# Optimization experiments

Hardware: AMD Instinct MI355X
Metric: run time of the kernel (lower is better)

Reference implementation:

```python
import jax, jax.numpy as jnp
import numpy as np

H, C = 4, 128            # heads, per-head channels (GATConv(in, 128, heads=4))
HC = H * C               # 512
NEG_SLOPE = 0.2          # PyG GATConv default LeakyReLU slope
EPS_BN = 1e-5


def gat_conv(x, src, dst, W, a_src, a_dst, b, n_nodes):
    # x: [N, F_in], W: [F_in, H*C], a_src/a_dst: [H, C], b: [H*C]
    h = (x @ W).reshape(n_nodes, H, C)                       # [N,H,C]
    al_s = jnp.einsum('nhc,hc->nh', h, a_src)                # [N,H]
    al_d = jnp.einsum('nhc,hc->nh', h, a_dst)                # [N,H]
    e = jax.nn.leaky_relu(al_s[src] + al_d[dst], NEG_SLOPE)  # [E,H] per-edge logits
    m = jax.ops.segment_max(e, dst, num_segments=n_nodes)    # stable segment softmax
    p = jnp.exp(e - m[dst])
    s = jax.ops.segment_sum(p, dst, num_segments=n_nodes)
    alpha = p / (s[dst] + 1e-16)                             # [E,H]
    out = jax.ops.segment_sum(h[src] * alpha[:, :, None], dst, num_segments=n_nodes)
    return out.reshape(n_nodes, HC) + b                      # concat heads + bias


def batch_norm(x, g, b):
    mu = x.mean(0)
    var = x.var(0)  # biased, as torch BatchNorm1d uses for normalization
    return (x - mu) * jax.lax.rsqrt(var + EPS_BN) * g + b


def setup_inputs() -> dict:
    N, E, F_IN, OUT = 20000, 256000, 128, 10
    key = jax.random.key(0)
    ks = jax.random.split(key, 40)
    sc = 0.05
    inp = {
        'x': jax.random.normal(ks[0], (N, F_IN), dtype=jnp.float32),
        'edge_index': jax.random.randint(ks[1], (2, E), 0, N, dtype=jnp.int64) if jax.config.jax_enable_x64 else jax.random.randint(ks[1], (2, E), 0, N).astype(jnp.int32),
        'batch': jnp.zeros((N,), dtype=jnp.int32),
    }
    k = 2
    fin = F_IN
    for i in range(1, 5):
        inp[f'W{i}'] = jax.random.normal(ks[k], (fin, HC), dtype=jnp.float32) * sc; k += 1
        inp[f'as{i}'] = jax.random.normal(ks[k], (H, C), dtype=jnp.float32) * sc; k += 1
        inp[f'ad{i}'] = jax.random.normal(ks[k], (H, C), dtype=jnp.float32) * sc; k += 1
        inp[f'b{i}'] = jnp.zeros((HC,), dtype=jnp.float32)
        inp[f'g{i}'] = jnp.ones((HC,), dtype=jnp.float32)
        inp[f'bt{i}'] = jnp.zeros((HC,), dtype=jnp.float32)
        fin = HC
    inp['lw1'] = jax.random.normal(ks[k], (HC, 128), dtype=jnp.float32) * sc; k += 1
    inp['lb1'] = jnp.zeros((128,), dtype=jnp.float32)
    inp['lw2'] = jax.random.normal(ks[k], (128, 64), dtype=jnp.float32) * sc; k += 1
    inp['lb2'] = jnp.zeros((64,), dtype=jnp.float32)
    inp['lw3'] = jax.random.normal(ks[k], (64, OUT), dtype=jnp.float32) * sc; k += 1
    inp['lb3'] = jnp.zeros((OUT,), dtype=jnp.float32)
    return inp


def reference(x, edge_index, batch,
              W1, as1, ad1, b1, g1, bt1,
              W2, as2, ad2, b2, g2, bt2,
              W3, as3, ad3, b3, g3, bt3,
              W4, as4, ad4, b4, g4, bt4,
              lw1, lb1, lw2, lb2, lw3, lb3):
    n = x.shape[0]
    # add self-loops (PyG GATConv default add_self_loops=True)
    loops = jnp.arange(n, dtype=edge_index.dtype)
    src = jnp.concatenate([edge_index[0], loops])
    dst = jnp.concatenate([edge_index[1], loops])

    h = jax.nn.elu(gat_conv(x, src, dst, W1, as1, ad1, b1, n))
    h = batch_norm(h, g1, bt1)
    h = jax.nn.elu(gat_conv(h, src, dst, W2, as2, ad2, b2, n))
    h = batch_norm(h, g2, bt2)
    h = jax.nn.elu(gat_conv(h, src, dst, W3, as3, ad3, b3, n))
    h = batch_norm(h, g3, bt3)
    h = jax.nn.elu(gat_conv(h, src, dst, W4, as4, ad4, b4, n))
    h = batch_norm(h, g4, bt4)

    h = jax.nn.relu(h @ lw1 + lb1)   # dropout is identity in eval
    h = jax.nn.relu(h @ lw2 + lb2)
    return jax.nn.log_softmax(h @ lw3 + lb3, axis=-1)
```

## Files before the change

### kernel.cpp

```cpp
#include <hip/hip_runtime.h>
#include <hip/hip_bf16.h>
#include <math.h>

#define HC 512
#define NHEAD 4
#define NEG_SLOPE 0.2f
#define EPS_BN 1e-5f

typedef __attribute__((ext_vector_type(8))) _Float16 half8;
typedef __attribute__((ext_vector_type(4))) _Float16 half4v;
typedef __attribute__((ext_vector_type(4))) float f32x4;

#define GLOAD16(gptr, lptr)                                                      \
    __builtin_amdgcn_global_load_lds(                                            \
        (const __attribute__((address_space(1))) unsigned int*)(gptr),           \
        (__attribute__((address_space(3))) unsigned int*)(lptr), 16, 0, 0)

__global__ void hist_kernel(const int* __restrict__ dstE, int* __restrict__ cnt,
                            int E, int N) {
    int i = blockIdx.x * 256 + threadIdx.x;
    if (i < E + N) {
        int d = (i < E) ? dstE[i] : (i - E);
        atomicAdd(&cnt[d], 1);
    }
}

__global__ __launch_bounds__(1024) void scan_kernel(int* __restrict__ rowptr,
                                                    int* __restrict__ wr, int n) {
    __shared__ int wsum[16];
    __shared__ int carry_s;
    int t = threadIdx.x, lane = t & 63, wv = t >> 6;
    if (t == 0) carry_s = 0;
    __syncthreads();
    for (int base = 0; base < n; base += 1024) {
        int v = (base + t < n) ? rowptr[base + t] : 0;
        int x = v;
#pragma unroll
        for (int off = 1; off < 64; off <<= 1) {
            int y = __shfl_up(x, off);
            if (lane >= off) x += y;
        }
        if (lane == 63) wsum[wv] = x;
        __syncthreads();
        if (wv == 0) {
            int s = (lane < 16) ? wsum[lane] : 0;
#pragma unroll
            for (int off = 1; off < 16; off <<= 1) {
                int y = __shfl_up(s, off);
                if (lane >= off) s += y;
            }
            if (lane < 16) wsum[lane] = s;
        }
        __syncthreads();
        int woff = (wv == 0) ? 0 : wsum[wv - 1];
        int tot = wsum[15];
        int carry = carry_s;
        if (base + t < n) {
            int excl = carry + woff + x - v;
            rowptr[base + t] = excl;
            wr[base + t] = excl;
        }
        __syncthreads();
        if (t == 1023) carry_s = carry + tot;
        __syncthreads();
    }
    if (threadIdx.x == 0) rowptr[n] = carry_s;
}

__global__ void scatter_kernel(const int* __restrict__ srcE,
                               const int* __restrict__ dstE,
                               int* __restrict__ wr, int* __restrict__ csrc,
                               int E, int N) {
    int i = blockIdx.x * 256 + threadIdx.x;
    if (i < E + N) {
        int d = (i < E) ? dstE[i] : (i - E);
        int s = (i < E) ? srcE[i] : (i - E);
        int p = atomicAdd(&wr[d], 1);
        csrc[p] = s;
    }
}

__global__ __launch_bounds__(256) void advec_kernel(const double* __restrict__ stats,
                                                    const float* __restrict__ g,
                                                    const float* __restrict__ bt,
                                                    float* __restrict__ avec,
                                                    float* __restrict__ dvec,
                                                    double invN) {
    int k = blockIdx.x * 256 + threadIdx.x;
    if (k >= HC) return;
    double mu = stats[k] * invN;
    double var = stats[HC + k] * invN - mu * mu;
    float a = g[k] * (float)rsqrt(var + (double)EPS_BN);
    avec[k] = a;
    dvec[k] = bt[k] - (float)mu * a;
}

__global__ __launch_bounds__(256) void wsplit_kernel(const float* __restrict__ W,
                                                     const float* __restrict__ avec,
                                                     _Float16* __restrict__ hiT,
                                                     int K, int Nc) {
    __shared__ float tile[32][33];
    int bx = blockIdx.x * 32;
    int by = blockIdx.y * 32;
    int tx = threadIdx.x & 31, ty = threadIdx.x >> 5;
#pragma unroll
    for (int r = 0; r < 32; r += 8)
        tile[ty + r][tx] = W[(size_t)(by + ty + r) * Nc + bx + tx];
    __syncthreads();
    int k = by + tx;
    float a = avec ? avec[k] : 1.f;
#pragma unroll
    for (int r = 0; r < 32; r += 8) {
        int n = bx + ty + r;
        hiT[(size_t)n * K + k] = (_Float16)(tile[tx][ty + r] * a);
    }
}

__global__ __launch_bounds__(256) void bvec_kernel(const float* __restrict__ W,
                                                   const float* __restrict__ dvec,
                                                   const float* __restrict__ extra,
                                                   float* __restrict__ bvec,
                                                   int K, int Nc) {
    int wv = (blockIdx.x * 256 + threadIdx.x) >> 6;
    int lane = threadIdx.x & 63;
    if (wv >= Nc) return;
    float s = 0.f;
    for (int k = lane; k < K; k += 64)
        s = fmaf(dvec[k], W[(size_t)k * Nc + wv], s);
#pragma unroll
    for (int off = 32; off; off >>= 1) s += __shfl_xor(s, off);
    if (lane == 0) bvec[wv] = s + (extra ? extra[wv] : 0.f);
}

__global__ __launch_bounds__(256) void xcvt_kernel(const float* __restrict__ x,
                                                   _Float16* __restrict__ xh, int total) {
    for (int i = blockIdx.x * 256 + threadIdx.x; i < total; i += gridDim.x * 256)
        xh[i] = (_Float16)x[i];
}

template <int EPI>
__global__ __launch_bounds__(256) void mfma_gemm(const _Float16* __restrict__ A,
                                                 const _Float16* __restrict__ BT,
                                                 const float* __restrict__ bvec,
                                                 _Float16* __restrict__ H16,
                                                 float* __restrict__ C,
                                                 int M, int K, int Nc) {
    __shared__ _Float16 sm[2 * 4096];
    _Float16* sA = sm;
    _Float16* sB = sm + 4096;

    const int nwg = gridDim.x * gridDim.y;
    const int orig = blockIdx.y * gridDim.x + blockIdx.x;
    const int q = nwg >> 3, r = nwg & 7;
    const int xcd = orig & 7, local = orig >> 3;
    const int wgid = (xcd < r ? xcd * (q + 1) : r * (q + 1) + (xcd - r) * q) + local;
    const int bxi = wgid % gridDim.x, byi = wgid / gridDim.x;

    const int tid = threadIdx.x;
    const int wid = tid >> 6, lane = tid & 63;
    const int wm = wid >> 1, wn = wid & 1;
    const int bm = byi * 128, bn = bxi * 128;

    const int rowl = lane >> 2;
    const int cole = (lane & 3) * 8;
    const int c0 = wid * 2;

    const int frow = lane & 15;
    const int fko = (lane >> 4) * 8;

    f32x4 acc[4][4] = {};

    for (int k0 = 0; k0 < K; k0 += 32) {
#pragma unroll
        for (int cc = 0; cc < 2; ++cc) {
            int c = c0 + cc;
            int ra = bm + c * 16 + rowl; if (ra >= M) ra = M - 1;
            int rb = bn + c * 16 + rowl;
            GLOAD16(A + (size_t)ra * K + k0 + cole, &sA[c * 512]);
            GLOAD16(BT + (size_t)rb * K + k0 + cole, &sB[c * 512]);
        }
        __syncthreads();

        half8 av[4], bv[4];
#pragma unroll
        for (int mi = 0; mi < 4; ++mi) {
            int rr = wm * 64 + mi * 16 + frow;
            av[mi] = *(const half8*)&sA[rr * 32 + fko];
        }
#pragma unroll
        for (int ni = 0; ni < 4; ++ni) {
            int rr = wn * 64 + ni * 16 + frow;
            bv[ni] = *(const half8*)&sB[rr * 32 + fko];
        }
#pragma unroll
        for (int mi = 0; mi < 4; ++mi)
#pragma unroll
            for (int ni = 0; ni < 4; ++ni)
                acc[mi][ni] = __builtin_amdgcn_mfma_f32_16x16x32_f16(av[mi], bv[ni], acc[mi][ni], 0, 0, 0);
        __syncthreads();
    }

    const int crow = (lane >> 4) * 4;
    const int ccol = lane & 15;
#pragma unroll
    for (int mi = 0; mi < 4; ++mi)
#pragma unroll
        for (int ni = 0; ni < 4; ++ni) {
            int gc = bn + wn * 64 + ni * 16 + ccol;
            float bvv = bvec[gc];
#pragma unroll
            for (int rr = 0; rr < 4; ++rr) {
                int gr = bm + wm * 64 + mi * 16 + crow + rr;
                if (gr >= M) continue;
                float v = acc[mi][ni][rr] + bvv;
                if (EPI == 0) {
                    H16[(size_t)gr * Nc + gc] = (_Float16)v;
                } else {
                    C[(size_t)gr * Nc + gc] = fmaxf(v, 0.f);
                }
            }
        }
}

template <int BM, int BN, int BK, int TM, int TN, int EPI>
__global__ __launch_bounds__(256) void gemm_k(const float* __restrict__ A,
                                              const float* __restrict__ B,
                                              const float* __restrict__ bias,
                                              float* __restrict__ C,
                                              int M, int K, int N) {
    constexpr int PAD = 4;
    __shared__ float sA[BK][BM + PAD];
    __shared__ float sB[BK][BN];

    const int tid = threadIdx.x;
    const int bm = blockIdx.y * BM, bn = blockIdx.x * BN;
    constexpr int TX = BN / TN;
    const int tx = tid % TX, ty = tid / TX;

    float acc[TM][TN] = {};

    constexpr int AF4 = BK / 4;
    const int a4 = tid % AF4;
    const int ar0 = tid / AF4;
    constexpr int AROWS = 256 / AF4;
    constexpr int APASS = BM / AROWS;

    constexpr int BF4 = BN / 4;
    const int b4 = tid % BF4;
    const int br0 = tid / BF4;
    constexpr int BROWS = 256 / BF4;
    constexpr int BPASS = BK / BROWS;

    for (int kt = 0; kt < K; kt += BK) {
        __syncthreads();
#pragma unroll
        for (int p = 0; p < APASS; ++p) {
            int row = ar0 + p * AROWS;
            int gr = bm + row;
            if (gr >= M) gr = M - 1;
            float4 v = *(const float4*)&A[(size_t)gr * K + kt + a4 * 4];
            sA[a4 * 4 + 0][row] = v.x;
            sA[a4 * 4 + 1][row] = v.y;
            sA[a4 * 4 + 2][row] = v.z;
            sA[a4 * 4 + 3][row] = v.w;
        }
#pragma unroll
        for (int p = 0; p < BPASS; ++p) {
            int row = br0 + p * BROWS;
            float4 v = *(const float4*)&B[(size_t)(kt + row) * N + bn + b4 * 4];
            *(float4*)&sB[row][b4 * 4] = v;
        }
        __syncthreads();
#pragma unroll
        for (int k = 0; k < BK; ++k) {
            float ar[TM], br[TN];
#pragma unroll
            for (int i = 0; i < TM; i += 4)
                *(float4*)&ar[i] = *(const float4*)&sA[k][ty * TM + i];
#pragma unroll
            for (int j = 0; j < TN; j += 4)
                *(float4*)&br[j] = *(const float4*)&sB[k][tx * TN + j];
#pragma unroll
            for (int i = 0; i < TM; ++i)
#pragma unroll
                for (int j = 0; j < TN; ++j)
                    acc[i][j] = fmaf(ar[i], br[j], acc[i][j]);
        }
    }

#pragma unroll
    for (int i = 0; i < TM; ++i) {
        int r = bm + ty * TM + i;
        if (r >= M) continue;
#pragma unroll
        for (int j = 0; j < TN; j += 4) {
            int c = bn + tx * TN + j;
            float4 v;
            v.x = acc[i][j + 0]; v.y = acc[i][j + 1];
            v.z = acc[i][j + 2]; v.w = acc[i][j + 3];
            if (EPI == 1) {
                v.x = fmaxf(v.x + bias[c + 0], 0.f);
                v.y = fmaxf(v.y + bias[c + 1], 0.f);
                v.z = fmaxf(v.z + bias[c + 2], 0.f);
                v.w = fmaxf(v.w + bias[c + 3], 0.f);
            }
            *(float4*)&C[(size_t)r * N + c] = v;
        }
    }
}

__global__ __launch_bounds__(256) void al_kernel(const _Float16* __restrict__ h16,
                                                 const float* __restrict__ asrc,
                                                 const float* __restrict__ adst,
                                                 float* __restrict__ al_s,
                                                 float* __restrict__ al_d, int N) {
    int wid = (blockIdx.x * 256 + threadIdx.x) >> 6;
    int lane = threadIdx.x & 63;
    if (wid >= N) return;
    half8 hv = *(const half8*)(h16 + (size_t)wid * HC + lane * 8);
    float ss = 0.f, sd = 0.f;
#pragma unroll
    for (int j = 0; j < 8; ++j) {
        float v = (float)hv[j];
        ss = fmaf(v, asrc[lane * 8 + j], ss);
        sd = fmaf(v, adst[lane * 8 + j], sd);
    }
#pragma unroll
    for (int off = 8; off; off >>= 1) {
        ss += __shfl_xor(ss, off);
        sd += __shfl_xor(sd, off);
    }
    if ((lane & 15) == 0) {
        al_s[wid * NHEAD + (lane >> 4)] = ss;
        al_d[wid * NHEAD + (lane >> 4)] = sd;
    }
}

__global__ __launch_bounds__(256) void attw_kernel(const float* __restrict__ al_s,
                                                   const float* __restrict__ al_d,
                                                   const int* __restrict__ rowptr,
                                                   const int* __restrict__ csrc,
                                                   float4* __restrict__ alpha, int N) {
    int node = (blockIdx.x * 256 + threadIdx.x) >> 6;
    int lane = threadIdx.x & 63;
    if (node >= N) return;
    int e0 = rowptr[node], e1 = rowptr[node + 1];
    int deg = e1 - e0;
    float4 ad4 = *(const float4*)&al_d[node * NHEAD];

    if (deg <= 64) {
        float x0 = -INFINITY, x1 = -INFINITY, x2 = -INFINITY, x3 = -INFINITY;
        if (lane < deg) {
            int s = csrc[e0 + lane];
            float4 a = *(const float4*)&al_s[s * NHEAD];
            x0 = a.x + ad4.x; x0 = (x0 > 0.f) ? x0 : NEG_SLOPE * x0;
            x1 = a.y + ad4.y; x1 = (x1 > 0.f) ? x1 : NEG_SLOPE * x1;
            x2 = a.z + ad4.z; x2 = (x2 > 0.f) ? x2 : NEG_SLOPE * x2;
            x3 = a.w + ad4.w; x3 = (x3 > 0.f) ? x3 : NEG_SLOPE * x3;
        }
        float m0 = x0, m1 = x1, m2 = x2, m3 = x3;
#pragma unroll
        for (int off = 32; off; off >>= 1) {
            m0 = fmaxf(m0, __shfl_xor(m0, off));
            m1 = fmaxf(m1, __shfl_xor(m1, off));
            m2 = fmaxf(m2, __shfl_xor(m2, off));
            m3 = fmaxf(m3, __shfl_xor(m3, off));
        }
        float p0 = (lane < deg) ? __expf(x0 - m0) : 0.f;
        float p1 = (lane < deg) ? __expf(x1 - m1) : 0.f;
        float p2 = (lane < deg) ? __expf(x2 - m2) : 0.f;
        float p3 = (lane < deg) ? __expf(x3 - m3) : 0.f;
        float s0 = p0, s1 = p1, s2 = p2, s3 = p3;
#pragma unroll
        for (int off = 32; off; off >>= 1) {
            s0 += __shfl_xor(s0, off);
            s1 += __shfl_xor(s1, off);
            s2 += __shfl_xor(s2, off);
            s3 += __shfl_xor(s3, off);
        }
        if (lane < deg) {
            float4 w;
            w.x = p0 / (s0 + 1e-16f);
            w.y = p1 / (s1 + 1e-16f);
            w.z = p2 / (s2 + 1e-16f);
            w.w = p3 / (s3 + 1e-16f);
            alpha[e0 + lane] = w;
        }
        return;
    }

    float m0 = -INFINITY, m1 = -INFINITY, m2 = -INFINITY, m3 = -INFINITY;
    for (int i = e0 + lane; i < e1; i += 64) {
        int s = csrc[i];
        float4 a = *(const float4*)&al_s[s * NHEAD];
        float e;
        e = a.x + ad4.x; e = (e > 0.f) ? e : NEG_SLOPE * e; m0 = fmaxf(m0, e);
        e = a.y + ad4.y; e = (e > 0.f) ? e : NEG_SLOPE * e; m1 = fmaxf(m1, e);
        e = a.z + ad4.z; e = (e > 0.f) ? e : NEG_SLOPE * e; m2 = fmaxf(m2, e);
        e = a.w + ad4.w; e = (e > 0.f) ? e : NEG_SLOPE * e; m3 = fmaxf(m3, e);
    }
#pragma unroll
    for (int off = 32; off; off >>= 1) {
        m0 = fmaxf(m0, __shfl_xor(m0, off));
        m1 = fmaxf(m1, __shfl_xor(m1, off));
        m2 = fmaxf(m2, __shfl_xor(m2, off));
        m3 = fmaxf(m3, __shfl_xor(m3, off));
    }
    float s0 = 0, s1 = 0, s2 = 0, s3 = 0;
    for (int i = e0 + lane; i < e1; i += 64) {
        int s = csrc[i];
        float4 a = *(const float4*)&al_s[s * NHEAD];
        float e;
        e = a.x + ad4.x; e = (e > 0.f) ? e : NEG_SLOPE * e; s0 += __expf(e - m0);
        e = a.y + ad4.y; e = (e > 0.f) ? e : NEG_SLOPE * e; s1 += __expf(e - m1);
        e = a.z + ad4.z; e = (e > 0.f) ? e : NEG_SLOPE * e; s2 += __expf(e - m2);
        e = a.w + ad4.w; e = (e > 0.f) ? e : NEG_SLOPE * e; s3 += __expf(e - m3);
    }
#pragma unroll
    for (int off = 32; off; off >>= 1) {
        s0 += __shfl_xor(s0, off);
        s1 += __shfl_xor(s1, off);
        s2 += __shfl_xor(s2, off);
        s3 += __shfl_xor(s3, off);
    }
    float r0 = 1.f / (s0 + 1e-16f), r1 = 1.f / (s1 + 1e-16f);
    float r2 = 1.f / (s2 + 1e-16f), r3 = 1.f / (s3 + 1e-16f);
    for (int i = e0 + lane; i < e1; i += 64) {
        int s = csrc[i];
        float4 a = *(const float4*)&al_s[s * NHEAD];
        float4 w;
        float e;
        e = a.x + ad4.x; e = (e > 0.f) ? e : NEG_SLOPE * e; w.x = __expf(e - m0) * r0;
        e = a.y + ad4.y; e = (e > 0.f) ? e : NEG_SLOPE * e; w.y = __expf(e - m1) * r1;
        e = a.z + ad4.z; e = (e > 0.f) ? e : NEG_SLOPE * e; w.z = __expf(e - m2) * r2;
        e = a.w + ad4.w; e = (e > 0.f) ? e : NEG_SLOPE * e; w.w = __expf(e - m3) * r3;
        alpha[i] = w;
    }
}

__global__ __launch_bounds__(256) void gath_kernel(const _Float16* __restrict__ h16,
                                                   const float4* __restrict__ alpha,
                                                   const int* __restrict__ rowptr,
                                                   const int* __restrict__ csrc,
                                                   const float* __restrict__ bias,
                                                   _Float16* __restrict__ out16, int N) {
    int gid = blockIdx.x * 256 + threadIdx.x;
    int wv = gid >> 6, lane = gid & 63;
    int node = wv >> 1, hf = wv & 1;
    if (node >= N) return;
    int e0 = rowptr[node], e1 = rowptr[node + 1];
    size_t cb = (size_t)(hf * 256 + lane * 4);
    bool hiHead = (lane & 32) != 0;

#define PICKW(q) (hf ? (hiHead ? (q).w : (q).z) : (hiHead ? (q).y : (q).x))

    float a0 = 0, a1 = 0, a2 = 0, a3 = 0;
    int i = e0;
    for (; i + 4 <= e1; i += 4) {
        int s0 = csrc[i], s1 = csrc[i + 1], s2 = csrc[i + 2], s3 = csrc[i + 3];
        float4 q0 = alpha[i], q1 = alpha[i + 1], q2 = alpha[i + 2], q3 = alpha[i + 3];
        half4v v0 = *(const half4v*)(h16 + (size_t)s0 * HC + cb);
        half4v v1 = *(const half4v*)(h16 + (size_t)s1 * HC + cb);
        half4v v2 = *(const half4v*)(h16 + (size_t)s2 * HC + cb);
        half4v v3 = *(const half4v*)(h16 + (size_t)s3 * HC + cb);
        float w0 = PICKW(q0), w1 = PICKW(q1), w2 = PICKW(q2), w3 = PICKW(q3);
        a0 = fmaf((float)v0[0], w0, a0); a1 = fmaf((float)v0[1], w0, a1);
        a2 = fmaf((float)v0[2], w0, a2); a3 = fmaf((float)v0[3], w0, a3);
        a0 = fmaf((float)v1[0], w1, a0); a1 = fmaf((float)v1[1], w1, a1);
        a2 = fmaf((float)v1[2], w1, a2); a3 = fmaf((float)v1[3], w1, a3);
        a0 = fmaf((float)v2[0], w2, a0); a1 = fmaf((float)v2[1], w2, a1);
        a2 = fmaf((float)v2[2], w2, a2); a3 = fmaf((float)v2[3], w2, a3);
        a0 = fmaf((float)v3[0], w3, a0); a1 = fmaf((float)v3[1], w3, a1);
        a2 = fmaf((float)v3[2], w3, a2); a3 = fmaf((float)v3[3], w3, a3);
    }
    for (; i < e1; ++i) {
        int s = csrc[i];
        float4 q = alpha[i];
        float w = PICKW(q);
        half4v v = *(const half4v*)(h16 + (size_t)s * HC + cb);
        a0 = fmaf((float)v[0], w, a0); a1 = fmaf((float)v[1], w, a1);
        a2 = fmaf((float)v[2], w, a2); a3 = fmaf((float)v[3], w, a3);
    }
#undef PICKW

    float4 bb = *(const float4*)&bias[cb];
    a0 += bb.x; a1 += bb.y; a2 += bb.z; a3 += bb.w;
    a0 = (a0 > 0.f) ? a0 : (__expf(a0) - 1.f);
    a1 = (a1 > 0.f) ? a1 : (__expf(a1) - 1.f);
    a2 = (a2 > 0.f) ? a2 : (__expf(a2) - 1.f);
    a3 = (a3 > 0.f) ? a3 : (__expf(a3) - 1.f);
    half4v o = {(_Float16)a0, (_Float16)a1, (_Float16)a2, (_Float16)a3};
    *(half4v*)(out16 + (size_t)node * HC + cb) = o;
}

__global__ __launch_bounds__(256) void bnstat_kernel(const _Float16* __restrict__ x,
                                                     double* __restrict__ partials,
                                                     int N) {
    __shared__ double lds[2][4][HC];
    int t = threadIdx.x;
    int lane = t & 63, wv = t >> 6;
    int c0 = lane * 8;
    const int stride = gridDim.x * 4;

    float s[8] = {}, q[8] = {};
    int r = blockIdx.x * 4 + wv;
    for (; r + stride < N; r += 2 * stride) {
        half8 v0 = *(const half8*)&x[(size_t)r * HC + c0];
        half8 v1 = *(const half8*)&x[(size_t)(r + stride) * HC + c0];
#pragma unroll
        for (int j = 0; j < 8; ++j) {
            float f0 = (float)v0[j], f1 = (float)v1[j];
            s[j] += f0 + f1;
            q[j] = fmaf(f0, f0, q[j]);
            q[j] = fmaf(f1, f1, q[j]);
        }
    }
    for (; r < N; r += stride) {
        half8 v0 = *(const half8*)&x[(size_t)r * HC + c0];
#pragma unroll
        for (int j = 0; j < 8; ++j) {
            float f0 = (float)v0[j];
            s[j] += f0;
            q[j] = fmaf(f0, f0, q[j]);
        }
    }
#pragma unroll
    for (int j = 0; j < 8; ++j) {
        lds[0][wv][c0 + j] = (double)s[j];
        lds[1][wv][c0 + j] = (double)q[j];
    }
    __syncthreads();
    if (wv == 0) {
        double* pb = partials + (size_t)blockIdx.x * 1024;
#pragma unroll
        for (int j = 0; j < 8; ++j) {
            int c = c0 + j;
            pb[c] = lds[0][0][c] + lds[0][1][c] + lds[0][2][c] + lds[0][3][c];
            pb[512 + c] = lds[1][0][c] + lds[1][1][c] + lds[1][2][c] + lds[1][3][c];
        }
    }
}

__global__ __launch_bounds__(256) void bnred_kernel(const double* __restrict__ partials,
                                                    double* __restrict__ stats, int nb) {
    int wv = (blockIdx.x * 256 + threadIdx.x) >> 6;
    int lane = threadIdx.x & 63;
    if (wv >= 1024) return;
    double s = 0.0;
    for (int b = lane; b < nb; b += 64)
        s += partials[(size_t)b * 1024 + wv];
#pragma unroll
    for (int off = 32; off; off >>= 1) s += __shfl_xor(s, off);
    if (lane == 0) stats[wv] = s;
}

__global__ __launch_bounds__(256) void head_kernel(const float* __restrict__ x,
                                                   const float* __restrict__ w,
                                                   const float* __restrict__ b,
                                                   float* __restrict__ out, int N) {
    int wid = (blockIdx.x * 256 + threadIdx.x) >> 6;
    int lane = threadIdx.x & 63;
    if (wid >= N) return;
    float v = x[(size_t)wid * 64 + lane];
    float my = -INFINITY;
#pragma unroll
    for (int j = 0; j < 10; ++j) {
        float t = v * w[lane * 10 + j];
#pragma unroll
        for (int off = 32; off; off >>= 1) t += __shfl_xor(t, off);
        t += b[j];
        if (lane == j) my = t;
    }
    float mx = my;
#pragma unroll
    for (int off = 32; off; off >>= 1) mx = fmaxf(mx, __shfl_xor(mx, off));
    float p = (lane < 10) ? expf(my - mx) : 0.f;
    float sum = p;
#pragma unroll
    for (int off = 32; off; off >>= 1) sum += __shfl_xor(sum, off);
    if (lane < 10) out[(size_t)wid * 10 + lane] = my - mx - logf(sum);
}

extern "C" void kernel_launch(void* const* d_in, const int* in_sizes, int n_in,
                              void* d_out, int out_size, void* d_ws, size_t ws_size,
                              hipStream_t stream) {
    const float* x = (const float*)d_in[0];
    const int* ei = (const int*)d_in[1];
    const int N = in_sizes[0] / 128;
    const int E = in_sizes[1] / 2;
    const int EN = E + N;
    const int NB_STAT = 256;

    double* stats = (double*)d_ws;
    double* partials = stats + 1024;
    float* als   = (float*)(partials + (size_t)NB_STAT * 1024);
    float* ald   = als + (size_t)N * NHEAD;
    float4* alpha = (float4*)(ald + (size_t)N * NHEAD);
    float* bvec  = (float*)(alpha + EN);
    float* avec  = bvec + 512;
    float* dvec  = avec + 512;
    float* m1    = dvec + 512;
    float* m2    = m1 + (size_t)N * 128;
    _Float16* xh   = (_Float16*)(m2 + (size_t)N * 64);
    _Float16* h16  = xh + (size_t)N * 128;
    _Float16* out16 = h16 + (size_t)N * HC;
    _Float16* wpool = out16 + (size_t)N * HC;
    _Float16* wthi[4], * wtmhi;
    _Float16* p = wpool;
    wthi[0] = p; p += 512 * 128;
    for (int L = 1; L < 4; ++L) { wthi[L] = p; p += 512 * 512; }
    wtmhi = p; p += 128 * 512;
    int* rowptr = (int*)p;
    int* wr = rowptr + (N + 1);
    int* csrc = wr + N;

    hipMemsetAsync(rowptr, 0, (N + 1) * sizeof(int), stream);
    hist_kernel<<<(EN + 255) / 256, 256, 0, stream>>>(ei + E, rowptr, E, N);
    scan_kernel<<<1, 1024, 0, stream>>>(rowptr, wr, N);
    scatter_kernel<<<(EN + 255) / 256, 256, 0, stream>>>(ei, ei + E, wr, csrc, E, N);

    wsplit_kernel<<<dim3(512 / 32, 128 / 32), 256, 0, stream>>>(
        (const float*)d_in[3], nullptr, wthi[0], 128, 512);
    xcvt_kernel<<<1024, 256, 0, stream>>>(x, xh, N * 128);
    hipMemsetAsync(bvec, 0, 512 * sizeof(float), stream);

    const int nodeBlocks = (N * 64 + 255) / 256;
    const int gathBlocks = (N * 128 + 255) / 256;
    const double invN = 1.0 / (double)N;

    for (int L = 0; L < 4; ++L) {
        const float* as_ = (const float*)d_in[4 + 6 * L];
        const float* ad_ = (const float*)d_in[5 + 6 * L];
        const float* b_  = (const float*)d_in[6 + 6 * L];
        const float* g_  = (const float*)d_in[7 + 6 * L];
        const float* bt_ = (const float*)d_in[8 + 6 * L];
        const _Float16* Ain = (L == 0) ? xh : out16;
        const int curK = (L == 0) ? 128 : 512;

        mfma_gemm<0><<<dim3(HC / 128, (N + 127) / 128), 256, 0, stream>>>(
            Ain, wthi[L], bvec, h16, nullptr, N, curK, HC);
        al_kernel<<<nodeBlocks, 256, 0, stream>>>(h16, as_, ad_, als, ald, N);
        attw_kernel<<<nodeBlocks, 256, 0, stream>>>(als, ald, rowptr, csrc, alpha, N);
        gath_kernel<<<gathBlocks, 256, 0, stream>>>(h16, alpha, rowptr, csrc, b_,
                                                    out16, N);
        bnstat_kernel<<<NB_STAT, 256, 0, stream>>>(out16, partials, N);
        bnred_kernel<<<256, 256, 0, stream>>>(partials, stats, NB_STAT);
        advec_kernel<<<2, 256, 0, stream>>>(stats, g_, bt_, avec, dvec, invN);

        if (L < 3) {
            const float* Wn = (const float*)d_in[3 + 6 * (L + 1)];
            wsplit_kernel<<<dim3(512 / 32, 512 / 32), 256, 0, stream>>>(
                Wn, avec, wthi[L + 1], 512, 512);
            bvec_kernel<<<(512 * 64 + 255) / 256, 256, 0, stream>>>(
                Wn, dvec, nullptr, bvec, 512, 512);
        } else {
            const float* lw1 = (const float*)d_in[27];
            const float* lb1 = (const float*)d_in[28];
            wsplit_kernel<<<dim3(128 / 32, 512 / 32), 256, 0, stream>>>(
                lw1, avec, wtmhi, 512, 128);
            bvec_kernel<<<(128 * 64 + 255) / 256, 256, 0, stream>>>(
                lw1, dvec, lb1, bvec, 512, 128);
        }
    }

    const float* lw2 = (const float*)d_in[29];
    const float* lb2 = (const float*)d_in[30];
    const float* lw3 = (const float*)d_in[31];
    const float* lb3 = (const float*)d_in[32];

    mfma_gemm<1><<<dim3(1, (N + 127) / 128), 256, 0, stream>>>(
        out16, wtmhi, bvec, nullptr, m1, N, 512, 128);
    gemm_k<64, 64, 16, 4, 4, 1><<<dim3(1, (N + 63) / 64), 256, 0, stream>>>(
        m1, lw2, lb2, m2, N, 128, 64);
    head_kernel<<<nodeBlocks, 256, 0, stream>>>(m2, lw3, lb3, (float*)d_out, N);
}
```

Baseline: 638.4 us.

## Fuse attention softmax into gather kernel and merge BN reduce with affine

Merges the per-edge attention softmax kernel into the neighbor gather kernel. For low-degree nodes one wave computes alpha into shared memory, and the two half-channel waves of each node consume it after a block barrier. High-degree nodes still spill alpha to global memory. Separately, the BN partial reduction and the scale/shift computation are folded into one kernel. Together these remove two launches per layer and the global alpha round trip for most edges, at the cost of a __syncthreads and one idle wave per node during the softmax phase.

```diff
diff --git a/kernel.cpp b/kernel.cpp
--- a/kernel.cpp
+++ b/kernel.cpp
@@ -78,21 +78,6 @@
         int p = atomicAdd(&wr[d], 1);
         csrc[p] = s;
     }
-}
-
-__global__ __launch_bounds__(256) void advec_kernel(const double* __restrict__ stats,
-                                                    const float* __restrict__ g,
-                                                    const float* __restrict__ bt,
-                                                    float* __restrict__ avec,
-                                                    float* __restrict__ dvec,
-                                                    double invN) {
-    int k = blockIdx.x * 256 + threadIdx.x;
-    if (k >= HC) return;
-    double mu = stats[k] * invN;
-    double var = stats[HC + k] * invN - mu * mu;
-    float a = g[k] * (float)rsqrt(var + (double)EPS_BN);
-    avec[k] = a;
-    dvec[k] = bt[k] - (float)mu * a;
 }
 
 __global__ __launch_bounds__(256) void wsplit_kernel(const float* __restrict__ W,
@@ -336,152 +321,183 @@
     }
 }
 
-__global__ __launch_bounds__(256) void attw_kernel(const float* __restrict__ al_s,
-                                                   const float* __restrict__ al_d,
-                                                   const int* __restrict__ rowptr,
-                                                   const int* __restrict__ csrc,
-                                                   float4* __restrict__ alpha, int N) {
-    int node = (blockIdx.x * 256 + threadIdx.x) >> 6;
-    int lane = threadIdx.x & 63;
-    if (node >= N) return;
-    int e0 = rowptr[node], e1 = rowptr[node + 1];
-    int deg = e1 - e0;
-    float4 ad4 = *(const float4*)&al_d[node * NHEAD];
-
-    if (deg <= 64) {
-        float x0 = -INFINITY, x1 = -INFINITY, x2 = -INFINITY, x3 = -INFINITY;
-        if (lane < deg) {
-            int s = csrc[e0 + lane];
-            float4 a = *(const float4*)&al_s[s * NHEAD];
-            x0 = a.x + ad4.x; x0 = (x0 > 0.f) ? x0 : NEG_SLOPE * x0;
-            x1 = a.y + ad4.y; x1 = (x1 > 0.f) ? x1 : NEG_SLOPE * x1;
-            x2 = a.z + ad4.z; x2 = (x2 > 0.f) ? x2 : NEG_SLOPE * x2;
-            x3 = a.w + ad4.w; x3 = (x3 > 0.f) ? x3 : NEG_SLOPE * x3;
-        }
-        float m0 = x0, m1 = x1, m2 = x2, m3 = x3;
-#pragma unroll
-        for (int off = 32; off; off >>= 1) {
-            m0 = fmaxf(m0, __shfl_xor(m0, off));
-            m1 = fmaxf(m1, __shfl_xor(m1, off));
-            m2 = fmaxf(m2, __shfl_xor(m2, off));
-            m3 = fmaxf(m3, __shfl_xor(m3, off));
-        }
-        float p0 = (lane < deg) ? __expf(x0 - m0) : 0.f;
-        float p1 = (lane < deg) ? __expf(x1 - m1) : 0.f;
-        float p2 = (lane < deg) ? __expf(x2 - m2) : 0.f;
-        float p3 = (lane < deg) ? __expf(x3 - m3) : 0.f;
-        float s0 = p0, s1 = p1, s2 = p2, s3 = p3;
-#pragma unroll
-        for (int off = 32; off; off >>= 1) {
-            s0 += __shfl_xor(s0, off);
-            s1 += __shfl_xor(s1, off);
-            s2 += __shfl_xor(s2, off);
-            s3 += __shfl_xor(s3, off);
-        }
-        if (lane < deg) {
-            float4 w;
-            w.x = p0 / (s0 + 1e-16f);
-            w.y = p1 / (s1 + 1e-16f);
-            w.z = p2 / (s2 + 1e-16f);
-            w.w = p3 / (s3 + 1e-16f);
-            alpha[e0 + lane] = w;
-        }
-        return;
-    }
-
-    float m0 = -INFINITY, m1 = -INFINITY, m2 = -INFINITY, m3 = -INFINITY;
-    for (int i = e0 + lane; i < e1; i += 64) {
-        int s = csrc[i];
-        float4 a = *(const float4*)&al_s[s * NHEAD];
-        float e;
-        e = a.x + ad4.x; e = (e > 0.f) ? e : NEG_SLOPE * e; m0 = fmaxf(m0, e);
-        e = a.y + ad4.y; e = (e > 0.f) ? e : NEG_SLOPE * e; m1 = fmaxf(m1, e);
-        e = a.z + ad4.z; e = (e > 0.f) ? e : NEG_SLOPE * e; m2 = fmaxf(m2, e);
-        e = a.w + ad4.w; e = (e > 0.f) ? e : NEG_SLOPE * e; m3 = fmaxf(m3, e);
-    }
-#pragma unroll
-    for (int off = 32; off; off >>= 1) {
-        m0 = fmaxf(m0, __shfl_xor(m0, off));
-        m1 = fmaxf(m1, __shfl_xor(m1, off));
-        m2 = fmaxf(m2, __shfl_xor(m2, off));
-        m3 = fmaxf(m3, __shfl_xor(m3, off));
-    }
-    float s0 = 0, s1 = 0, s2 = 0, s3 = 0;
-    for (int i = e0 + lane; i < e1; i += 64) {
-        int s = csrc[i];
-        float4 a = *(const float4*)&al_s[s * NHEAD];
-        float e;
-        e = a.x + ad4.x; e = (e > 0.f) ? e : NEG_SLOPE * e; s0 += __expf(e - m0);
-        e = a.y + ad4.y; e = (e > 0.f) ? e : NEG_SLOPE * e; s1 += __expf(e - m1);
-        e = a.z + ad4.z; e = (e > 0.f) ? e : NEG_SLOPE * e; s2 += __expf(e - m2);
-        e = a.w + ad4.w; e = (e > 0.f) ? e : NEG_SLOPE * e; s3 += __expf(e - m3);
-    }
-#pragma unroll
-    for (int off = 32; off; off >>= 1) {
-        s0 += __shfl_xor(s0, off);
-        s1 += __shfl_xor(s1, off);
-        s2 += __shfl_xor(s2, off);
-        s3 += __shfl_xor(s3, off);
-    }
-    float r0 = 1.f / (s0 + 1e-16f), r1 = 1.f / (s1 + 1e-16f);
-    float r2 = 1.f / (s2 + 1e-16f), r3 = 1.f / (s3 + 1e-16f);
-    for (int i = e0 + lane; i < e1; i += 64) {
-        int s = csrc[i];
-        float4 a = *(const float4*)&al_s[s * NHEAD];
-        float4 w;
-        float e;
-        e = a.x + ad4.x; e = (e > 0.f) ? e : NEG_SLOPE * e; w.x = __expf(e - m0) * r0;
-        e = a.y + ad4.y; e = (e > 0.f) ? e : NEG_SLOPE * e; w.y = __expf(e - m1) * r1;
-        e = a.z + ad4.z; e = (e > 0.f) ? e : NEG_SLOPE * e; w.z = __expf(e - m2) * r2;
-        e = a.w + ad4.w; e = (e > 0.f) ? e : NEG_SLOPE * e; w.w = __expf(e - m3) * r3;
-        alpha[i] = w;
-    }
-}
-
-__global__ __launch_bounds__(256) void gath_kernel(const _Float16* __restrict__ h16,
-                                                   const float4* __restrict__ alpha,
-                                                   const int* __restrict__ rowptr,
-                                                   const int* __restrict__ csrc,
-                                                   const float* __restrict__ bias,
-                                                   _Float16* __restrict__ out16, int N) {
+__global__ __launch_bounds__(256) void attgath_kernel(const _Float16* __restrict__ h16,
+                                                      const float* __restrict__ al_s,
+                                                      const float* __restrict__ al_d,
+                                                      const int* __restrict__ rowptr,
+                                                      const int* __restrict__ csrc,
+                                                      float4* __restrict__ galpha,
+                                                      const float* __restrict__ bias,
+                                                      _Float16* __restrict__ out16,
+                                                      int N) {
+    __shared__ float4 lal[2][64];
     int gid = blockIdx.x * 256 + threadIdx.x;
     int wv = gid >> 6, lane = gid & 63;
     int node = wv >> 1, hf = wv & 1;
-    if (node >= N) return;
-    int e0 = rowptr[node], e1 = rowptr[node + 1];
+    int slot = (threadIdx.x >> 7);
+    bool valid = node < N;
+    int e0 = 0, deg = 0;
+    if (valid) {
+        e0 = rowptr[node];
+        deg = rowptr[node + 1] - e0;
+    }
+
+    if (valid && hf == 0) {
+        float4 ad4 = *(const float4*)&al_d[node * NHEAD];
+        if (deg <= 64) {
+            float x0 = -INFINITY, x1 = -INFINITY, x2 = -INFINITY, x3 = -INFINITY;
+            if (lane < deg) {
+                int s = csrc[e0 + lane];
+                float4 a = *(const float4*)&al_s[s * NHEAD];
+                x0 = a.x + ad4.x; x0 = (x0 > 0.f) ? x0 : NEG_SLOPE * x0;
+                x1 = a.y + ad4.y; x1 = (x1 > 0.f) ? x1 : NEG_SLOPE * x1;
+                x2 = a.z + ad4.z; x2 = (x2 > 0.f) ? x2 : NEG_SLOPE * x2;
+                x3 = a.w + ad4.w; x3 = (x3 > 0.f) ? x3 : NEG_SLOPE * x3;
+            }
+            float m0 = x0, m1 = x1, m2 = x2, m3 = x3;
+#pragma unroll
+            for (int off = 32; off; off >>= 1) {
+                m0 = fmaxf(m0, __shfl_xor(m0, off));
+                m1 = fmaxf(m1, __shfl_xor(m1, off));
+                m2 = fmaxf(m2, __shfl_xor(m2, off));
+                m3 = fmaxf(m3, __shfl_xor(m3, off));
+            }
+            float p0 = (lane < deg) ? __expf(x0 - m0) : 0.f;
+            float p1 = (lane < deg) ? __expf(x1 - m1) : 0.f;
+            float p2 = (lane < deg) ? __expf(x2 - m2) : 0.f;
+            float p3 = (lane < deg) ? __expf(x3 - m3) : 0.f;
+            float s0 = p0, s1 = p1, s2 = p2, s3 = p3;
+#pragma unroll
+            for (int off = 32; off; off >>= 1) {
+                s0 += __shfl_xor(s0, off);
+                s1 += __shfl_xor(s1, off);
+                s2 += __shfl_xor(s2, off);
+                s3 += __shfl_xor(s3, off);
+            }
+            if (lane < deg) {
+                float4 w;
+                w.x = p0 / (s0 + 1e-16f);
+                w.y = p1 / (s1 + 1e-16f);
+                w.z = p2 / (s2 + 1e-16f);
+                w.w = p3 / (s3 + 1e-16f);
+                lal[slot][lane] = w;
+            }
+        } else {
+            int e1 = e0 + deg;
+            float m0 = -INFINITY, m1 = -INFINITY, m2 = -INFINITY, m3 = -INFINITY;
+            for (int i = e0 + lane; i < e1; i += 64) {
+                int s = csrc[i];
+                float4 a = *(const float4*)&al_s[s * NHEAD];
+                float e;
+                e = a.x + ad4.x; e = (e > 0.f) ? e : NEG_SLOPE * e; m0 = fmaxf(m0, e);
+                e = a.y + ad4.y; e = (e > 0.f) ? e : NEG_SLOPE * e; m1 = fmaxf(m1, e);
+                e = a.z + ad4.z; e = (e > 0.f) ? e : NEG_SLOPE * e; m2 = fmaxf(m2, e);
+                e = a.w + ad4.w; e = (e > 0.f) ? e : NEG_SLOPE * e; m3 = fmaxf(m3, e);
+            }
+#pragma unroll
+            for (int off = 32; off; off >>= 1) {
+                m0 = fmaxf(m0, __shfl_xor(m0, off));
+                m1 = fmaxf(m1, __shfl_xor(m1, off));
+                m2 = fmaxf(m2, __shfl_xor(m2, off));
+                m3 = fmaxf(m3, __shfl_xor(m3, off));
+            }
+            float s0 = 0, s1 = 0, s2 = 0, s3 = 0;
+            for (int i = e0 + lane; i < e1; i += 64) {
+                int s = csrc[i];
+                float4 a = *(const float4*)&al_s[s * NHEAD];
+                float e;
+                e = a.x + ad4.x; e = (e > 0.f) ? e : NEG_SLOPE * e; s0 += __expf(e - m0);
+                e = a.y + ad4.y; e = (e > 0.f) ? e : NEG_SLOPE * e; s1 += __expf(e - m1);
+                e = a.z + ad4.z; e = (e > 0.f) ? e : NEG_SLOPE * e; s2 += __expf(e - m2);
+                e = a.w + ad4.w; e = (e > 0.f) ? e : NEG_SLOPE * e; s3 += __expf(e - m3);
+            }
+#pragma unroll
+            for (int off = 32; off; off >>= 1) {
+                s0 += __shfl_xor(s0, off);
+                s1 += __shfl_xor(s1, off);
+                s2 += __shfl_xor(s2, off);
+                s3 += __shfl_xor(s3, off);
+            }
+            float r0 = 1.f / (s0 + 1e-16f), r1 = 1.f / (s1 + 1e-16f);
+            float r2 = 1.f / (s2 + 1e-16f), r3 = 1.f / (s3 + 1e-16f);
+            for (int i = e0 + lane; i < e1; i += 64) {
+                int s = csrc[i];
+                float4 a = *(const float4*)&al_s[s * NHEAD];
+                float4 w;
+                float e;
+                e = a.x + ad4.x; e = (e > 0.f) ? e : NEG_SLOPE * e; w.x = __expf(e - m0) * r0;
+                e = a.y + ad4.y; e = (e > 0.f) ? e : NEG_SLOPE * e; w.y = __expf(e - m1) * r1;
+                e = a.z + ad4.z; e = (e > 0.f) ? e : NEG_SLOPE * e; w.z = __expf(e - m2) * r2;
+                e = a.w + ad4.w; e = (e > 0.f) ? e : NEG_SLOPE * e; w.w = __expf(e - m3) * r3;
+                galpha[i] = w;
+            }
+        }
+    }
+    __syncthreads();
+    if (!valid) return;
+
     size_t cb = (size_t)(hf * 256 + lane * 4);
     bool hiHead = (lane & 32) != 0;
-
-#define PICKW(q) (hf ? (hiHead ? (q).w : (q).z) : (hiHead ? (q).y : (q).x))
+    int comp = hf * 2 + (hiHead ? 1 : 0);
+    const float* lap = (const float*)&lal[slot][0] + comp;
 
     float a0 = 0, a1 = 0, a2 = 0, a3 = 0;
-    int i = e0;
-    for (; i + 4 <= e1; i += 4) {
-        int s0 = csrc[i], s1 = csrc[i + 1], s2 = csrc[i + 2], s3 = csrc[i + 3];
-        float4 q0 = alpha[i], q1 = alpha[i + 1], q2 = alpha[i + 2], q3 = alpha[i + 3];
-        half4v v0 = *(const half4v*)(h16 + (size_t)s0 * HC + cb);
-        half4v v1 = *(const half4v*)(h16 + (size_t)s1 * HC + cb);
-        half4v v2 = *(const half4v*)(h16 + (size_t)s2 * HC + cb);
-        half4v v3 = *(const half4v*)(h16 + (size_t)s3 * HC + cb);
-        float w0 = PICKW(q0), w1 = PICKW(q1), w2 = PICKW(q2), w3 = PICKW(q3);
-        a0 = fmaf((float)v0[0], w0, a0); a1 = fmaf((float)v0[1], w0, a1);
-        a2 = fmaf((float)v0[2], w0, a2); a3 = fmaf((float)v0[3], w0, a3);
-        a0 = fmaf((float)v1[0], w1, a0); a1 = fmaf((float)v1[1], w1, a1);
-        a2 = fmaf((float)v1[2], w1, a2); a3 = fmaf((float)v1[3], w1, a3);
-        a0 = fmaf((float)v2[0], w2, a0); a1 = fmaf((float)v2[1], w2, a1);
-        a2 = fmaf((float)v2[2], w2, a2); a3 = fmaf((float)v2[3], w2, a3);
-        a0 = fmaf((float)v3[0], w3, a0); a1 = fmaf((float)v3[1], w3, a1);
-        a2 = fmaf((float)v3[2], w3, a2); a3 = fmaf((float)v3[3], w3, a3);
-    }
-    for (; i < e1; ++i) {
-        int s = csrc[i];
-        float4 q = alpha[i];
-        float w = PICKW(q);
-        half4v v = *(const half4v*)(h16 + (size_t)s * HC + cb);
-        a0 = fmaf((float)v[0], w, a0); a1 = fmaf((float)v[1], w, a1);
-        a2 = fmaf((float)v[2], w, a2); a3 = fmaf((float)v[3], w, a3);
-    }
-#undef PICKW
+    if (deg <= 64) {
+        int i = 0;
+        for (; i + 4 <= deg; i += 4) {
+            int s0 = csrc[e0 + i], s1 = csrc[e0 + i + 1];
+            int s2 = csrc[e0 + i + 2], s3 = csrc[e0 + i + 3];
+            float w0 = lap[4 * i], w1 = lap[4 * (i + 1)];
+            float w2 = lap[4 * (i + 2)], w3 = lap[4 * (i + 3)];
+            half4v v0 = *(const half4v*)(h16 + (size_t)s0 * HC + cb);
+            half4v v1 = *(const half4v*)(h16 + (size_t)s1 * HC + cb);
+            half4v v2 = *(const half4v*)(h16 + (size_t)s2 * HC + cb);
+            half4v v3 = *(const half4v*)(h16 + (size_t)s3 * HC + cb);
+            a0 = fmaf((float)v0[0], w0, a0); a1 = fmaf((float)v0[1], w0, a1);
+            a2 = fmaf((float)v0[2], w0, a2); a3 = fmaf((float)v0[3], w0, a3);
+            a0 = fmaf((float)v1[0], w1, a0); a1 = fmaf((float)v1[1], w1, a1);
+            a2 = fmaf((float)v1[2], w1, a2); a3 = fmaf((float)v1[3], w1, a3);
+            a0 = fmaf((float)v2[0], w2, a0); a1 = fmaf((float)v2[1], w2, a1);
+            a2 = fmaf((float)v2[2], w2, a2); a3 = fmaf((float)v2[3], w2, a3);
+            a0 = fmaf((float)v3[0], w3, a0); a1 = fmaf((float)v3[1], w3, a1);
+            a2 = fmaf((float)v3[2], w3, a2); a3 = fmaf((float)v3[3], w3, a3);
+        }
+        for (; i < deg; ++i) {
+            int s = csrc[e0 + i];
+            float w = lap[4 * i];
+            half4v v = *(const half4v*)(h16 + (size_t)s * HC + cb);
+            a0 = fmaf((float)v[0], w, a0); a1 = fmaf((float)v[1], w, a1);
+            a2 = fmaf((float)v[2], w, a2); a3 = fmaf((float)v[3], w, a3);
+        }
+    } else {
+        const float* gap = (const float*)&galpha[e0] + comp;
+        int i = 0;
+        for (; i + 4 <= deg; i += 4) {
+            int s0 = csrc[e0 + i], s1 = csrc[e0 + i + 1];
+            int s2 = csrc[e0 + i + 2], s3 = csrc[e0 + i + 3];
+            float w0 = gap[4 * i], w1 = gap[4 * (i + 1)];
+            float w2 = gap[4 * (i + 2)], w3 = gap[4 * (i + 3)];
+            half4v v0 = *(const half4v*)(h16 + (size_t)s0 * HC + cb);
+            half4v v1 = *(const half4v*)(h16 + (size_t)s1 * HC + cb);
+            half4v v2 = *(const half4v*)(h16 + (size_t)s2 * HC + cb);
+            half4v v3 = *(const half4v*)(h16 + (size_t)s3 * HC + cb);
+            a0 = fmaf((float)v0[0], w0, a0); a1 = fmaf((float)v0[1], w0, a1);
+            a2 = fmaf((float)v0[2], w0, a2); a3 = fmaf((float)v0[3], w0, a3);
+            a0 = fmaf((float)v1[0], w1, a0); a1 = fmaf((float)v1[1], w1, a1);
+            a2 = fmaf((float)v1[2], w1, a2); a3 = fmaf((float)v1[3], w1, a3);
+            a0 = fmaf((float)v2[0], w2, a0); a1 = fmaf((float)v2[1], w2, a1);
+            a2 = fmaf((float)v2[2], w2, a2); a3 = fmaf((float)v2[3], w2, a3);
+            a0 = fmaf((float)v3[0], w3, a0); a1 = fmaf((float)v3[1], w3, a1);
+            a2 = fmaf((float)v3[2], w3, a2); a3 = fmaf((float)v3[3], w3, a3);
+        }
+        for (; i < deg; ++i) {
+            int s = csrc[e0 + i];
+            float w = gap[4 * i];
+            half4v v = *(const half4v*)(h16 + (size_t)s * HC + cb);
+            a0 = fmaf((float)v[0], w, a0); a1 = fmaf((float)v[1], w, a1);
+            a2 = fmaf((float)v[2], w, a2); a3 = fmaf((float)v[3], w, a3);
+        }
+    }
 
     float4 bb = *(const float4*)&bias[cb];
     a0 += bb.x; a1 += bb.y; a2 += bb.z; a3 += bb.w;
@@ -541,17 +557,32 @@
     }
 }
 
-__global__ __launch_bounds__(256) void bnred_kernel(const double* __restrict__ partials,
-                                                    double* __restrict__ stats, int nb) {
-    int wv = (blockIdx.x * 256 + threadIdx.x) >> 6;
+__global__ __launch_bounds__(256) void bnadv_kernel(const double* __restrict__ partials,
+                                                    const float* __restrict__ g,
+                                                    const float* __restrict__ bt,
+                                                    float* __restrict__ avec,
+                                                    float* __restrict__ dvec,
+                                                    int nb, double invN) {
+    int c = (blockIdx.x * 256 + threadIdx.x) >> 6;
     int lane = threadIdx.x & 63;
-    if (wv >= 1024) return;
-    double s = 0.0;
-    for (int b = lane; b < nb; b += 64)
-        s += partials[(size_t)b * 1024 + wv];
-#pragma unroll
-    for (int off = 32; off; off >>= 1) s += __shfl_xor(s, off);
-    if (lane == 0) stats[wv] = s;
+    if (c >= HC) return;
+    double s = 0.0, qq = 0.0;
+    for (int b = lane; b < nb; b += 64) {
+        s += partials[(size_t)b * 1024 + c];
+        qq += partials[(size_t)b * 1024 + 512 + c];
+    }
+#pragma unroll
+    for (int off = 32; off; off >>= 1) {
+        s += __shfl_xor(s, off);
+        qq += __shfl_xor(qq, off);
+    }
+    if (lane == 0) {
+        double mu = s * invN;
+        double var = qq * invN - mu * mu;
+        float a = g[c] * (float)rsqrt(var + (double)EPS_BN);
+        avec[c] = a;
+        dvec[c] = bt[c] - (float)mu * a;
+    }
 }
 
 __global__ __launch_bounds__(256) void head_kernel(const float* __restrict__ x,
@@ -591,12 +622,11 @@
     const int EN = E + N;
     const int NB_STAT = 256;
 
-    double* stats = (double*)d_ws;
-    double* partials = stats + 1024;
+    double* partials = (double*)d_ws;
     float* als   = (float*)(partials + (size_t)NB_STAT * 1024);
     float* ald   = als + (size_t)N * NHEAD;
-    float4* alpha = (float4*)(ald + (size_t)N * NHEAD);
-    float* bvec  = (float*)(alpha + EN);
+    float4* galpha = (float4*)(ald + (size_t)N * NHEAD);
+    float* bvec  = (float*)(galpha + EN);
     float* avec  = bvec + 512;
     float* dvec  = avec + 512;
     float* m1    = dvec + 512;
@@ -640,12 +670,11 @@
         mfma_gemm<0><<<dim3(HC / 128, (N + 127) / 128), 256, 0, stream>>>(
             Ain, wthi[L], bvec, h16, nullptr, N, curK, HC);
         al_kernel<<<nodeBlocks, 256, 0, stream>>>(h16, as_, ad_, als, ald, N);
-        attw_kernel<<<nodeBlocks, 256, 0, stream>>>(als, ald, rowptr, csrc, alpha, N);
-        gath_kernel<<<gathBlocks, 256, 0, stream>>>(h16, alpha, rowptr, csrc, b_,
-                                                    out16, N);
+        attgath_kernel<<<gathBlocks, 256, 0, stream>>>(h16, als, ald, rowptr, csrc,
+                                                       galpha, b_, out16, N);
         bnstat_kernel<<<NB_STAT, 256, 0, stream>>>(out16, partials, N);
-        bnred_kernel<<<256, 256, 0, stream>>>(partials, stats, NB_STAT);
-        advec_kernel<<<2, 256, 0, stream>>>(stats, g_, bt_, avec, dvec, invN);
+        bnadv_kernel<<<(HC * 64 + 255) / 256, 256, 0, stream>>>(
+            partials, g_, bt_, avec, dvec, NB_STAT, invN);
 
         if (L < 3) {
             const float* Wn = (const float*)d_in[3 + 6 * (L + 1)];
```

Result: faster. 594.3 us (-6.9%).
